# Kernel tuning notes

Measured on AMD Instinct MI355X. Metric: run time of the kernel, lower is better.

Reference implementation:

```python
import jax, jax.numpy as jnp
import numpy as np

N, E, F_IN, H, D, K = 50000, 800000, 128, 128, 64, 4

def setup_inputs():
    key = jax.random.key(0)
    ks = jax.random.split(key, 10)
    def rnd(k, shape, s=0.05):
        return jax.random.normal(k, shape, dtype=jnp.float32) * s
    return {
        "x": jax.random.normal(ks[0], (N, F_IN), dtype=jnp.float32),
        "edge_index": jax.random.randint(ks[1], (2, E), 0, N, dtype=jnp.int32),
        "W1": rnd(ks[2], (F_IN, H)),
        "b1": jnp.zeros((H,), jnp.float32),
        "a1": jnp.full((), 0.25, jnp.float32),
        "W2": rnd(ks[3], (H, H)),
        "b2": jnp.zeros((H,), jnp.float32),
        "a2": jnp.full((), 0.25, jnp.float32),
        "Wmu": rnd(ks[4], (K, H, D)),
        "bmu": jnp.zeros((K, D), jnp.float32),
        "amu": jnp.full((K,), 0.25, jnp.float32),
        "Wlv": rnd(ks[5], (K, H, D)),
        "blv": jnp.zeros((K, D), jnp.float32),
        "alv": jnp.full((K,), 0.25, jnp.float32),
        "Wr": rnd(ks[6], (K, D)),
        "br": jnp.zeros((K,), jnp.float32),
        "eps": jax.random.normal(ks[7], (N, K * D), dtype=jnp.float32),
    }

def _prelu(v, a):
    return jnp.where(v >= 0, v, a * v)

def _gcn_norm(edge_index):
    # PyG GCNConv defaults: add self-loops, symmetric deg^{-1/2} normalization
    loop = jnp.arange(N, dtype=edge_index.dtype)
    src = jnp.concatenate([edge_index[0], loop])
    dst = jnp.concatenate([edge_index[1], loop])
    deg = jax.ops.segment_sum(jnp.ones_like(dst, jnp.float32), dst, num_segments=N)
    dinv = jnp.where(deg > 0, jax.lax.rsqrt(deg), 0.0)
    norm = dinv[src] * dinv[dst]  # per-edge coefficient
    return src, dst, norm

def reference(x, edge_index, W1, b1, a1, W2, b2, a2, Wmu, bmu, amu, Wlv, blv, alv, Wr, br, eps):
    src, dst, norm = _gcn_norm(edge_index)
    def prop(h):  # gather -> normalize -> scatter-add
        return jax.ops.segment_sum(h[src] * norm[:, None], dst, num_segments=N)
    # shared GCN stack: GCNConv = propagate(x @ W) + b, then PReLU
    h = _prelu(prop(x @ W1) + b1, a1)
    hgcn = _prelu(prop(h @ W2) + b2, a2)
    # per-branch GCNConvs share the input; propagation is linear, so
    # propagate(hgcn @ Wk) == propagate(hgcn) @ Wk -> propagate once for all K
    p = prop(hgcn)  # (N, H)
    mu_k = _prelu(jnp.einsum('nh,khd->knd', p, Wmu) + bmu[:, None, :], amu[:, None, None])  # (K,N,D)
    lv_k = jax.nn.sigmoid(_prelu(jnp.einsum('nh,khd->knd', p, Wlv) + blv[:, None, :], alv[:, None, None]))
    mu = jnp.transpose(mu_k, (1, 0, 2)).reshape(N, K * D)
    logvar = jnp.transpose(lv_k, (1, 0, 2)).reshape(N, K * D)
    hk = eps * jnp.exp(0.5 * logvar) + mu  # reparameterize
    r = jax.nn.sigmoid(jnp.einsum('nkd,kd->nk', hk.reshape(N, K, D), Wr) + br)  # (N,K)
    return hgcn, logvar, mu, hk, r
```

## Files before the change

### kernel.cpp

```cpp
#include <hip/hip_runtime.h>
#include <math.h>

#define N_NODES 50000
#define N_EDGES 800000
#define HDIM 128
#define KD 256

typedef float f32x4 __attribute__((ext_vector_type(4)));
typedef short s16x8 __attribute__((ext_vector_type(8)));

__device__ __forceinline__ ushort f2b(float f) {
    union { float f; unsigned u; } x; x.f = f;
    unsigned u = x.u;
    return (ushort)((u + 0x7FFF + ((u >> 16) & 1)) >> 16);
}
__device__ __forceinline__ float b2f(ushort h) {
    union { unsigned u; float f; } x; x.u = ((unsigned)h) << 16; return x.f;
}

__global__ void zero_int(int* __restrict__ p, int n) {
    int i = blockIdx.x * blockDim.x + threadIdx.x;
    if (i < n) p[i] = 0;
}

__global__ void count_deg(const int* __restrict__ dst, int* __restrict__ cnt, int e) {
    int i = blockIdx.x * blockDim.x + threadIdx.x;
    if (i < e) atomicAdd(&cnt[dst[i]], 1);
}

__global__ void calc_dinv(const int* __restrict__ cnt, float* __restrict__ dinv, int n) {
    int i = blockIdx.x * blockDim.x + threadIdx.x;
    if (i < n) dinv[i] = rsqrtf((float)(cnt[i] + 1));
}

__global__ __launch_bounds__(1024)
void scan_blk(const int* __restrict__ cnt, int* __restrict__ offsets,
              int* __restrict__ blocksum, int n) {
    __shared__ int wsum[16];
    int tid = threadIdx.x;
    int i = blockIdx.x * 1024 + tid;
    int lane = tid & 63, wid = tid >> 6;
    int v = (i < n) ? cnt[i] : 0;
    int x = v;
    #pragma unroll
    for (int off = 1; off < 64; off <<= 1) {
        int t = __shfl_up(x, off, 64);
        if (lane >= off) x += t;
    }
    if (lane == 63) wsum[wid] = x;
    __syncthreads();
    if (wid == 0) {
        int w = (lane < 16) ? wsum[lane] : 0;
        #pragma unroll
        for (int off = 1; off < 16; off <<= 1) {
            int t = __shfl_up(w, off, 64);
            if (lane >= off) w += t;
        }
        if (lane < 16) wsum[lane] = w;
    }
    __syncthreads();
    int waveoff = (wid > 0) ? wsum[wid - 1] : 0;
    if (i < n) offsets[i] = x + waveoff - v;
    if (tid == 1023) blocksum[blockIdx.x] = x + waveoff;
}

__global__ void scan_top(const int* __restrict__ blocksum, int* __restrict__ blockpref,
                         int* __restrict__ offsets, int nb, int n) {
    int lane = threadIdx.x;
    int v = (lane < nb) ? blocksum[lane] : 0;
    int x = v;
    #pragma unroll
    for (int off = 1; off < 64; off <<= 1) {
        int t = __shfl_up(x, off, 64);
        if (lane >= off) x += t;
    }
    if (lane < nb) blockpref[lane] = x - v;
    if (lane == 63) offsets[n] = x;
}

__global__ __launch_bounds__(1024)
void scan_add(int* __restrict__ offsets, int* __restrict__ cursor,
              const int* __restrict__ blockpref, int n) {
    int i = blockIdx.x * 1024 + threadIdx.x;
    if (i < n) {
        int o = offsets[i] + blockpref[blockIdx.x];
        offsets[i] = o;
        cursor[i] = o;
    }
}

__global__ void fill_csr(const int* __restrict__ src, const int* __restrict__ dst,
                         int* __restrict__ cursor, int* __restrict__ csr, int e) {
    int i = blockIdx.x * blockDim.x + threadIdx.x;
    if (i < e) {
        int d = dst[i];
        int pos = atomicAdd(&cursor[d], 1);
        csr[pos] = src[i];
    }
}

__global__ void conv_x(const float4* __restrict__ x, ushort4* __restrict__ o,
                       const float* __restrict__ dinv, int n4) {
    int i = blockIdx.x * 256 + threadIdx.x;
    if (i >= n4) return;
    int row = i >> 5;
    float dv = dinv[row];
    float4 v = x[i];
    ushort4 u;
    u.x = f2b(v.x * dv); u.y = f2b(v.y * dv);
    u.z = f2b(v.z * dv); u.w = f2b(v.w * dv);
    o[i] = u;
}

__global__ void prep_w(const float* __restrict__ W1, const float* __restrict__ W2,
                       const float* __restrict__ Wmu, const float* __restrict__ Wlv,
                       ushort* __restrict__ w1t, ushort* __restrict__ w2t,
                       ushort* __restrict__ bt3) {
    int i = blockIdx.x * 256 + threadIdx.x;
    if (i < 16384) {
        int nn = i >> 7, k = i & 127;
        w1t[i] = f2b(W1[k * 128 + nn]);
    } else if (i < 32768) {
        int j = i - 16384; int nn = j >> 7, k = j & 127;
        w2t[j] = f2b(W2[k * 128 + nn]);
    } else if (i < 98304) {
        int j = i - 32768;
        int h = j & 127; int nk = j >> 7; int nn = nk & 127; int k = nk >> 7;
        float v = (nn < 64) ? Wmu[k * 8192 + h * 64 + nn]
                            : Wlv[k * 8192 + h * 64 + (nn - 64)];
        bt3[j] = f2b(v);
    }
}

__global__ __launch_bounds__(256)
void prop_b(const ushort* __restrict__ hin, ushort* __restrict__ hout,
            const int* __restrict__ csr, const int* __restrict__ offsets,
            const float* __restrict__ dinv, int n) {
    int gw = blockIdx.x * 4 + (threadIdx.x >> 6);
    if (gw >= n) return;
    int lane = threadIdx.x & 63;
    int grp = lane >> 4, gl = lane & 15;
    int coff = gl << 3;
    int beg = offsets[gw], end = offsets[gw + 1];
    float a0[8] = {0.f,0.f,0.f,0.f,0.f,0.f,0.f,0.f};
    float a1[8] = {0.f,0.f,0.f,0.f,0.f,0.f,0.f,0.f};
    for (int base = beg; base < end; base += 64) {
        int cnt = end - base; if (cnt > 64) cnt = 64;
        int sidx = (lane < cnt) ? csr[base + lane] : 0;
        int j = grp;
        for (; j + 4 < cnt; j += 8) {
            int s0 = __shfl(sidx, j, 64);
            int s1 = __shfl(sidx, j + 4, 64);
            s16x8 v0 = *(const s16x8*)(hin + (s0 << 7) + coff);
            s16x8 v1 = *(const s16x8*)(hin + (s1 << 7) + coff);
            #pragma unroll
            for (int q = 0; q < 8; ++q) {
                a0[q] += b2f((ushort)v0[q]);
                a1[q] += b2f((ushort)v1[q]);
            }
        }
        if (j < cnt) {
            int s0 = __shfl(sidx, j, 64);
            s16x8 v0 = *(const s16x8*)(hin + (s0 << 7) + coff);
            #pragma unroll
            for (int q = 0; q < 8; ++q) a0[q] += b2f((ushort)v0[q]);
        }
    }
    #pragma unroll
    for (int q = 0; q < 8; ++q) {
        float t = a0[q] + a1[q];
        t += __shfl_xor(t, 16, 64);
        t += __shfl_xor(t, 32, 64);
        a0[q] = t;
    }
    if (grp == 0) {
        s16x8 sv = *(const s16x8*)(hin + (gw << 7) + coff);
        float dn = dinv[gw];
        s16x8 o;
        #pragma unroll
        for (int q = 0; q < 8; ++q) {
            float t = (a0[q] + b2f((ushort)sv[q])) * dn;
            o[q] = (short)f2b(t);
        }
        *(s16x8*)(hout + (gw << 7) + coff) = o;
    }
}

template<int MODE>
__global__ __launch_bounds__(256)
void gemm12(const ushort* __restrict__ A, const ushort* __restrict__ Bt,
            const float* __restrict__ bias, const float* __restrict__ alpha,
            const float* __restrict__ dinv,
            float* __restrict__ Cf, ushort* __restrict__ Cb, int nrows) {
    __shared__ char As[32768];
    __shared__ char Bs[32768];
    int tid = threadIdx.x;
    int row0 = blockIdx.x * 128;
    #pragma unroll
    for (int it = 0; it < 8; ++it) {
        int idx = tid + it * 256;
        int r = idx >> 4, cb = (idx & 15) << 4;
        int sw = cb ^ ((r & 15) << 4);
        uint4 v = make_uint4(0, 0, 0, 0);
        int row = row0 + r;
        if (row < nrows) v = *(const uint4*)((const char*)A + (size_t)row * 256 + cb);
        *(uint4*)(As + r * 256 + sw) = v;
        uint4 bv = *(const uint4*)((const char*)Bt + (size_t)idx * 16);
        *(uint4*)(Bs + r * 256 + sw) = bv;
    }
    __syncthreads();

    int w = tid >> 6, lane = tid & 63;
    int bq = lane >> 4, tr = lane & 15;
    f32x4 acc[2][8];
    #pragma unroll
    for (int mi = 0; mi < 2; ++mi)
        #pragma unroll
        for (int nj = 0; nj < 8; ++nj)
            acc[mi][nj] = (f32x4){0.f, 0.f, 0.f, 0.f};

    #pragma unroll
    for (int s = 0; s < 4; ++s) {
        int xoff = (s * 64 + bq * 16) ^ ((tr & 15) << 4);
        s16x8 af[2], bfr[8];
        #pragma unroll
        for (int mi = 0; mi < 2; ++mi)
            af[mi] = *(const s16x8*)(As + (w * 32 + mi * 16 + tr) * 256 + xoff);
        #pragma unroll
        for (int nj = 0; nj < 8; ++nj)
            bfr[nj] = *(const s16x8*)(Bs + (nj * 16 + tr) * 256 + xoff);
        #pragma unroll
        for (int mi = 0; mi < 2; ++mi)
            #pragma unroll
            for (int nj = 0; nj < 8; ++nj)
                acc[mi][nj] = __builtin_amdgcn_mfma_f32_16x16x32_bf16(af[mi], bfr[nj], acc[mi][nj], 0, 0, 0);
    }

    int g = lane >> 4, c = lane & 15;
    float aval = alpha[0];
    float bb[8];
    #pragma unroll
    for (int nj = 0; nj < 8; ++nj) bb[nj] = bias[nj * 16 + c];
    #pragma unroll
    for (int mi = 0; mi < 2; ++mi) {
        #pragma unroll
        for (int j = 0; j < 4; ++j) {
            int row = row0 + w * 32 + mi * 16 + g * 4 + j;
            if (row >= nrows) continue;
            float dv = dinv[row];
            #pragma unroll
            for (int nj = 0; nj < 8; ++nj) {
                int col = nj * 16 + c;
                float t = acc[mi][nj][j] + bb[nj];
                t = t >= 0.f ? t : aval * t;
                if (MODE) Cf[(size_t)row * 128 + col] = t;
                Cb[(size_t)row * 128 + col] = f2b(t * dv);
            }
        }
    }
}

template<int FUSED>
__global__ __launch_bounds__(256)
void gemm3(const ushort* __restrict__ A, const ushort* __restrict__ Bt3,
           const float* __restrict__ bmu, const float* __restrict__ blv,
           const float* __restrict__ amu, const float* __restrict__ alv,
           const float* __restrict__ Wr, const float* __restrict__ br,
           const float* __restrict__ eps,
           float* __restrict__ out_mu, float* __restrict__ out_lv,
           float* __restrict__ out_hk, float* __restrict__ out_r, int nrows) {
    __shared__ char As[32768];
    __shared__ char Bs[32768];
    int tid = threadIdx.x;
    int k = blockIdx.x;
    int row0 = blockIdx.y * 128;
    const ushort* Bt = Bt3 + (size_t)k * 16384;
    #pragma unroll
    for (int it = 0; it < 8; ++it) {
        int idx = tid + it * 256;
        int r = idx >> 4, cb = (idx & 15) << 4;
        int sw = cb ^ ((r & 15) << 4);
        uint4 v = make_uint4(0, 0, 0, 0);
        int row = row0 + r;
        if (row < nrows) v = *(const uint4*)((const char*)A + (size_t)row * 256 + cb);
        *(uint4*)(As + r * 256 + sw) = v;
        uint4 bv = *(const uint4*)((const char*)Bt + (size_t)idx * 16);
        *(uint4*)(Bs + r * 256 + sw) = bv;
    }
    __syncthreads();

    int w = tid >> 6, lane = tid & 63;
    int bq = lane >> 4, tr = lane & 15;
    f32x4 acc[2][8];
    #pragma unroll
    for (int mi = 0; mi < 2; ++mi)
        #pragma unroll
        for (int nj = 0; nj < 8; ++nj)
            acc[mi][nj] = (f32x4){0.f, 0.f, 0.f, 0.f};

    #pragma unroll
    for (int s = 0; s < 4; ++s) {
        int xoff = (s * 64 + bq * 16) ^ ((tr & 15) << 4);
        s16x8 af[2], bfr[8];
        #pragma unroll
        for (int mi = 0; mi < 2; ++mi)
            af[mi] = *(const s16x8*)(As + (w * 32 + mi * 16 + tr) * 256 + xoff);
        #pragma unroll
        for (int nj = 0; nj < 8; ++nj)
            bfr[nj] = *(const s16x8*)(Bs + (nj * 16 + tr) * 256 + xoff);
        #pragma unroll
        for (int mi = 0; mi < 2; ++mi)
            #pragma unroll
            for (int nj = 0; nj < 8; ++nj)
                acc[mi][nj] = __builtin_amdgcn_mfma_f32_16x16x32_bf16(af[mi], bfr[nj], acc[mi][nj], 0, 0, 0);
    }

    int g = lane >> 4, c = lane & 15;
    float amuv = amu[k], alvv = alv[k];
    float brk = br[k];
    float bmv[4], blvb[4], wrv[4];
    #pragma unroll
    for (int nj = 0; nj < 4; ++nj) {
        int d = nj * 16 + c;
        bmv[nj] = bmu[k * 64 + d];
        blvb[nj] = blv[k * 64 + d];
        wrv[nj] = FUSED ? Wr[k * 64 + d] : 0.f;
    }
    #pragma unroll
    for (int mi = 0; mi < 2; ++mi) {
        float rsum[4] = {0.f, 0.f, 0.f, 0.f};
        #pragma unroll
        for (int j = 0; j < 4; ++j) {
            int row = row0 + w * 32 + mi * 16 + g * 4 + j;
            if (row >= nrows) continue;
            #pragma unroll
            for (int nj = 0; nj < 4; ++nj) {
                int d = nj * 16 + c;
                size_t oc = (size_t)row * KD + k * 64 + d;
                float m_ = acc[mi][nj][j] + bmv[nj];
                m_ = m_ >= 0.f ? m_ : amuv * m_;
                float l_ = acc[mi][nj + 4][j] + blvb[nj];
                l_ = l_ >= 0.f ? l_ : alvv * l_;
                l_ = 1.f / (1.f + __expf(-l_));
                out_mu[oc] = m_;
                out_lv[oc] = l_;
                if (FUSED) {
                    float h = fmaf(eps[oc], __expf(0.5f * l_), m_);
                    out_hk[oc] = h;
                    rsum[j] = fmaf(h, wrv[nj], rsum[j]);
                }
            }
        }
        if (FUSED) {
            #pragma unroll
            for (int j = 0; j < 4; ++j) {
                float t = rsum[j];
                t += __shfl_xor(t, 1, 64);
                t += __shfl_xor(t, 2, 64);
                t += __shfl_xor(t, 4, 64);
                t += __shfl_xor(t, 8, 64);
                if (c == 0) {
                    int row = row0 + w * 32 + mi * 16 + g * 4 + j;
                    if (row < nrows)
                        out_r[(size_t)row * 4 + k] = 1.f / (1.f + __expf(-(t + brk)));
                }
            }
        }
    }
}

__global__ void hk_kernel(const float* __restrict__ mu, const float* __restrict__ lv,
                          const float* __restrict__ eps, const float* __restrict__ Wr,
                          const float* __restrict__ br, float* __restrict__ hk,
                          float* __restrict__ r, int n) {
    int gw = (blockIdx.x * blockDim.x + threadIdx.x) >> 6;
    int lane = threadIdx.x & 63;
    if (gw >= n) return;
    size_t base = (size_t)gw * KD;
    #pragma unroll
    for (int k = 0; k < 4; ++k) {
        int c = k * 64 + lane;
        float m = mu[base + c], v = lv[base + c], e = eps[base + c];
        float h = fmaf(e, __expf(0.5f * v), m);
        hk[base + c] = h;
        float t = h * Wr[k * 64 + lane];
        #pragma unroll
        for (int off = 32; off >= 1; off >>= 1) t += __shfl_xor(t, off, 64);
        if (lane == 0) r[(size_t)gw * 4 + k] = 1.f / (1.f + __expf(-(t + br[k])));
    }
}

extern "C" void kernel_launch(void* const* d_in, const int* in_sizes, int n_in,
                              void* d_out, int out_size, void* d_ws, size_t ws_size,
                              hipStream_t stream) {
    const float* x   = (const float*)d_in[0];
    const int*   ei  = (const int*)d_in[1];
    const float* W1  = (const float*)d_in[2];
    const float* b1  = (const float*)d_in[3];
    const float* a1  = (const float*)d_in[4];
    const float* W2  = (const float*)d_in[5];
    const float* b2  = (const float*)d_in[6];
    const float* a2  = (const float*)d_in[7];
    const float* Wmu = (const float*)d_in[8];
    const float* bmu = (const float*)d_in[9];
    const float* amu = (const float*)d_in[10];
    const float* Wlv = (const float*)d_in[11];
    const float* blv = (const float*)d_in[12];
    const float* alv = (const float*)d_in[13];
    const float* Wr  = (const float*)d_in[14];
    const float* br  = (const float*)d_in[15];
    const float* eps = (const float*)d_in[16];

    float* out      = (float*)d_out;
    float* out_hgcn = out;
    float* out_lv   = out + (size_t)N_NODES * HDIM;
    float* out_mu   = out_lv + (size_t)N_NODES * KD;
    float* out_hk   = out_mu + (size_t)N_NODES * KD;
    float* out_r    = out_hk + (size_t)N_NODES * KD;

    char* ws = (char*)d_ws;
    int*    cnt      = (int*)ws;
    int*    offsets  = (int*)(ws + 204800);
    int*    cursor   = (int*)(ws + 409600);
    int*    csr      = (int*)(ws + 614400);
    float*  dinv     = (float*)(ws + 3814400);
    ushort* w1t      = (ushort*)(ws + 4014592);
    ushort* w2t      = (ushort*)(ws + 4047360);
    ushort* bt3      = (ushort*)(ws + 4080128);
    int*    blocksum = (int*)(ws + 4211200);
    int*    blockpref= (int*)(ws + 4211456);

    ushort* S0 = (ushort*)out_hk;
    ushort* S1 = S0 + (size_t)N_NODES * HDIM;
    ushort* S2 = S1 + (size_t)N_NODES * HDIM;
    ushort* S3 = S2 + (size_t)N_NODES * HDIM;

    const size_t P_OFF = 4211712;
    const bool fused = ws_size >= P_OFF + (size_t)N_NODES * HDIM * 2;
    ushort* P = fused ? (ushort*)(ws + P_OFF) : S1;

    const int* e_src = ei;
    const int* e_dst = ei + N_EDGES;
    const int NB = (N_NODES + 1023) / 1024;

    zero_int <<<(N_NODES + 255) / 256, 256, 0, stream>>>(cnt, N_NODES);
    count_deg<<<(N_EDGES + 255) / 256, 256, 0, stream>>>(e_dst, cnt, N_EDGES);
    calc_dinv<<<(N_NODES + 255) / 256, 256, 0, stream>>>(cnt, dinv, N_NODES);
    scan_blk <<<NB, 1024, 0, stream>>>(cnt, offsets, blocksum, N_NODES);
    scan_top <<<1, 64, 0, stream>>>(blocksum, blockpref, offsets, NB, N_NODES);
    scan_add <<<NB, 1024, 0, stream>>>(offsets, cursor, blockpref, N_NODES);
    fill_csr <<<(N_EDGES + 255) / 256, 256, 0, stream>>>(e_src, e_dst, cursor, csr, N_EDGES);

    prep_w<<<384, 256, 0, stream>>>(W1, W2, Wmu, Wlv, w1t, w2t, bt3);
    conv_x<<<(N_NODES * 32 + 255) / 256, 256, 0, stream>>>((const float4*)x, (ushort4*)S0, dinv, N_NODES * 32);

    prop_b<<<12500, 256, 0, stream>>>(S0, S1, csr, offsets, dinv, N_NODES);
    gemm12<0><<<391, 256, 0, stream>>>(S1, w1t, b1, a1, dinv, nullptr, S2, N_NODES);
    prop_b<<<12500, 256, 0, stream>>>(S2, S3, csr, offsets, dinv, N_NODES);
    gemm12<1><<<391, 256, 0, stream>>>(S3, w2t, b2, a2, dinv, out_hgcn, S0, N_NODES);
    prop_b<<<12500, 256, 0, stream>>>(S0, P, csr, offsets, dinv, N_NODES);

    dim3 g3(4, 391);
    if (fused) {
        gemm3<1><<<g3, 256, 0, stream>>>(P, bt3, bmu, blv, amu, alv, Wr, br, eps,
                                         out_mu, out_lv, out_hk, out_r, N_NODES);
    } else {
        gemm3<0><<<g3, 256, 0, stream>>>(P, bt3, bmu, blv, amu, alv, Wr, br, eps,
                                         out_mu, out_lv, out_hk, out_r, N_NODES);
        hk_kernel<<<12500, 256, 0, stream>>>(out_mu, out_lv, eps, Wr, br, out_hk, out_r, N_NODES);
    }
}
```

Before: 291.7 us.

## Split propagation kernel across feature quarters with 16 edges per wavefront

The sparse gather-propagate kernel now uses a 2D grid where blockIdx.y picks a 32-column quarter of the 128-wide feature row. Each wavefront processes 16 edges at once, with 4 lanes per edge, instead of 4 edges with 16 lanes each. This gives more memory-level parallelism per wave and spreads the work over four times as many blocks, at the cost of 64-byte row segments per edge instead of full 256-byte rows. It also reads the CSR indices four times and adds two extra shuffle-reduction steps.

```diff
diff --git a/kernel.cpp b/kernel.cpp
--- a/kernel.cpp
+++ b/kernel.cpp
@@ -133,56 +133,44 @@
 }
 
 __global__ __launch_bounds__(256)
-void prop_b(const ushort* __restrict__ hin, ushort* __restrict__ hout,
+void prop_q(const ushort* __restrict__ hin, ushort* __restrict__ hout,
             const int* __restrict__ csr, const int* __restrict__ offsets,
             const float* __restrict__ dinv, int n) {
-    int gw = blockIdx.x * 4 + (threadIdx.x >> 6);
-    if (gw >= n) return;
+    int node = blockIdx.x * 4 + (threadIdx.x >> 6);
+    if (node >= n) return;
     int lane = threadIdx.x & 63;
-    int grp = lane >> 4, gl = lane & 15;
-    int coff = gl << 3;
-    int beg = offsets[gw], end = offsets[gw + 1];
-    float a0[8] = {0.f,0.f,0.f,0.f,0.f,0.f,0.f,0.f};
-    float a1[8] = {0.f,0.f,0.f,0.f,0.f,0.f,0.f,0.f};
+    int e = lane >> 2, il = lane & 3;
+    int eoff = blockIdx.y * 32 + (il << 3);
+    int beg = offsets[node], end = offsets[node + 1];
+    float acc[8] = {0.f,0.f,0.f,0.f,0.f,0.f,0.f,0.f};
     for (int base = beg; base < end; base += 64) {
         int cnt = end - base; if (cnt > 64) cnt = 64;
         int sidx = (lane < cnt) ? csr[base + lane] : 0;
-        int j = grp;
-        for (; j + 4 < cnt; j += 8) {
-            int s0 = __shfl(sidx, j, 64);
-            int s1 = __shfl(sidx, j + 4, 64);
-            s16x8 v0 = *(const s16x8*)(hin + (s0 << 7) + coff);
-            s16x8 v1 = *(const s16x8*)(hin + (s1 << 7) + coff);
-            #pragma unroll
-            for (int q = 0; q < 8; ++q) {
-                a0[q] += b2f((ushort)v0[q]);
-                a1[q] += b2f((ushort)v1[q]);
-            }
+        #pragma unroll 4
+        for (int j = e; j < cnt; j += 16) {
+            int s = __shfl(sidx, j, 64);
+            s16x8 v = *(const s16x8*)(hin + (s << 7) + eoff);
+            #pragma unroll
+            for (int q = 0; q < 8; ++q) acc[q] += b2f((ushort)v[q]);
         }
-        if (j < cnt) {
-            int s0 = __shfl(sidx, j, 64);
-            s16x8 v0 = *(const s16x8*)(hin + (s0 << 7) + coff);
-            #pragma unroll
-            for (int q = 0; q < 8; ++q) a0[q] += b2f((ushort)v0[q]);
-        }
     }
     #pragma unroll
     for (int q = 0; q < 8; ++q) {
-        float t = a0[q] + a1[q];
+        float t = acc[q];
+        t += __shfl_xor(t, 4, 64);
+        t += __shfl_xor(t, 8, 64);
         t += __shfl_xor(t, 16, 64);
         t += __shfl_xor(t, 32, 64);
-        a0[q] = t;
-    }
-    if (grp == 0) {
-        s16x8 sv = *(const s16x8*)(hin + (gw << 7) + coff);
-        float dn = dinv[gw];
+        acc[q] = t;
+    }
+    if (e == 0) {
+        s16x8 sv = *(const s16x8*)(hin + (node << 7) + eoff);
+        float dn = dinv[node];
         s16x8 o;
         #pragma unroll
-        for (int q = 0; q < 8; ++q) {
-            float t = (a0[q] + b2f((ushort)sv[q])) * dn;
-            o[q] = (short)f2b(t);
-        }
-        *(s16x8*)(hout + (gw << 7) + coff) = o;
+        for (int q = 0; q < 8; ++q)
+            o[q] = (short)f2b((acc[q] + b2f((ushort)sv[q])) * dn);
+        *(s16x8*)(hout + (node << 7) + eoff) = o;
     }
 }
 
@@ -454,11 +442,12 @@
     prep_w<<<384, 256, 0, stream>>>(W1, W2, Wmu, Wlv, w1t, w2t, bt3);
     conv_x<<<(N_NODES * 32 + 255) / 256, 256, 0, stream>>>((const float4*)x, (ushort4*)S0, dinv, N_NODES * 32);
 
-    prop_b<<<12500, 256, 0, stream>>>(S0, S1, csr, offsets, dinv, N_NODES);
+    dim3 gp(12500, 4);
+    prop_q<<<gp, 256, 0, stream>>>(S0, S1, csr, offsets, dinv, N_NODES);
     gemm12<0><<<391, 256, 0, stream>>>(S1, w1t, b1, a1, dinv, nullptr, S2, N_NODES);
-    prop_b<<<12500, 256, 0, stream>>>(S2, S3, csr, offsets, dinv, N_NODES);
+    prop_q<<<gp, 256, 0, stream>>>(S2, S3, csr, offsets, dinv, N_NODES);
     gemm12<1><<<391, 256, 0, stream>>>(S3, w2t, b2, a2, dinv, out_hgcn, S0, N_NODES);
-    prop_b<<<12500, 256, 0, stream>>>(S0, P, csr, offsets, dinv, N_NODES);
+    prop_q<<<gp, 256, 0, stream>>>(S0, P, csr, offsets, dinv, N_NODES);
 
     dim3 g3(4, 391);
     if (fused) {
```

Measured after the change: 432.9 us. +48.4%, slower.

## Switch gather intermediates to fp16, fp32 propagate outputs with split-bf16 GEMMs, sort CSR

Applied to the files above, without the earlier changes.

Gathered features are now stored as fp16 instead of bf16. Propagation outputs are written in fp32, and the GEMMs split each fp32 A value into hi and lo bf16 parts, issuing two MFMAs per tile, which recovers accuracy. A per-node insertion sort of the CSR neighbour lists is added, which may improve gather locality and makes summation order deterministic. The trade is more memory traffic on propagate outputs and GEMM inputs (fp32 instead of 16-bit), twice the MFMA work, 96KB of LDS per GEMM block, and an extra sort kernel. This looks aimed mainly at accuracy rather than speed.

```diff
diff --git a/kernel.cpp b/kernel.cpp
--- a/kernel.cpp
+++ b/kernel.cpp
@@ -16,6 +16,12 @@
 }
 __device__ __forceinline__ float b2f(ushort h) {
     union { unsigned u; float f; } x; x.u = ((unsigned)h) << 16; return x.f;
+}
+__device__ __forceinline__ ushort f2h(float f) {
+    union { _Float16 h; ushort u; } x; x.h = (_Float16)f; return x.u;
+}
+__device__ __forceinline__ float h2f(ushort u) {
+    union { ushort u; _Float16 h; } x; x.u = u; return (float)x.h;
 }
 
 __global__ void zero_int(int* __restrict__ p, int n) {
@@ -99,6 +105,18 @@
     }
 }
 
+__global__ void sort_csr(int* __restrict__ csr, const int* __restrict__ offsets, int n) {
+    int node = blockIdx.x * 256 + threadIdx.x;
+    if (node >= n) return;
+    int beg = offsets[node], end = offsets[node + 1];
+    for (int i = beg + 1; i < end; ++i) {
+        int key = csr[i];
+        int j = i - 1;
+        while (j >= beg && csr[j] > key) { csr[j + 1] = csr[j]; --j; }
+        csr[j + 1] = key;
+    }
+}
+
 __global__ void conv_x(const float4* __restrict__ x, ushort4* __restrict__ o,
                        const float* __restrict__ dinv, int n4) {
     int i = blockIdx.x * 256 + threadIdx.x;
@@ -107,8 +125,8 @@
     float dv = dinv[row];
     float4 v = x[i];
     ushort4 u;
-    u.x = f2b(v.x * dv); u.y = f2b(v.y * dv);
-    u.z = f2b(v.z * dv); u.w = f2b(v.w * dv);
+    u.x = f2h(v.x * dv); u.y = f2h(v.y * dv);
+    u.z = f2h(v.z * dv); u.w = f2h(v.w * dv);
     o[i] = u;
 }
 
@@ -133,7 +151,7 @@
 }
 
 __global__ __launch_bounds__(256)
-void prop_b(const ushort* __restrict__ hin, ushort* __restrict__ hout,
+void prop_b(const ushort* __restrict__ hin, float* __restrict__ hout,
             const int* __restrict__ csr, const int* __restrict__ offsets,
             const float* __restrict__ dinv, int n) {
     int gw = blockIdx.x * 4 + (threadIdx.x >> 6);
@@ -155,15 +173,15 @@
             s16x8 v1 = *(const s16x8*)(hin + (s1 << 7) + coff);
             #pragma unroll
             for (int q = 0; q < 8; ++q) {
-                a0[q] += b2f((ushort)v0[q]);
-                a1[q] += b2f((ushort)v1[q]);
+                a0[q] += h2f((ushort)v0[q]);
+                a1[q] += h2f((ushort)v1[q]);
             }
         }
         if (j < cnt) {
             int s0 = __shfl(sidx, j, 64);
             s16x8 v0 = *(const s16x8*)(hin + (s0 << 7) + coff);
             #pragma unroll
-            for (int q = 0; q < 8; ++q) a0[q] += b2f((ushort)v0[q]);
+            for (int q = 0; q < 8; ++q) a0[q] += h2f((ushort)v0[q]);
         }
     }
     #pragma unroll
@@ -176,23 +194,24 @@
     if (grp == 0) {
         s16x8 sv = *(const s16x8*)(hin + (gw << 7) + coff);
         float dn = dinv[gw];
-        s16x8 o;
-        #pragma unroll
-        for (int q = 0; q < 8; ++q) {
-            float t = (a0[q] + b2f((ushort)sv[q])) * dn;
-            o[q] = (short)f2b(t);
-        }
-        *(s16x8*)(hout + (gw << 7) + coff) = o;
+        float* orow = hout + (gw << 7) + coff;
+        float o[8];
+        #pragma unroll
+        for (int q = 0; q < 8; ++q)
+            o[q] = (a0[q] + h2f((ushort)sv[q])) * dn;
+        *(float4*)(orow)     = make_float4(o[0], o[1], o[2], o[3]);
+        *(float4*)(orow + 4) = make_float4(o[4], o[5], o[6], o[7]);
     }
 }
 
 template<int MODE>
 __global__ __launch_bounds__(256)
-void gemm12(const ushort* __restrict__ A, const ushort* __restrict__ Bt,
+void gemm12(const float* __restrict__ A, const ushort* __restrict__ Bt,
             const float* __restrict__ bias, const float* __restrict__ alpha,
             const float* __restrict__ dinv,
-            float* __restrict__ Cf, ushort* __restrict__ Cb, int nrows) {
-    __shared__ char As[32768];
+            float* __restrict__ Cf, ushort* __restrict__ Ch, int nrows) {
+    __shared__ char Ah[32768];
+    __shared__ char Al[32768];
     __shared__ char Bs[32768];
     int tid = threadIdx.x;
     int row0 = blockIdx.x * 128;
@@ -201,10 +220,24 @@
         int idx = tid + it * 256;
         int r = idx >> 4, cb = (idx & 15) << 4;
         int sw = cb ^ ((r & 15) << 4);
-        uint4 v = make_uint4(0, 0, 0, 0);
         int row = row0 + r;
-        if (row < nrows) v = *(const uint4*)((const char*)A + (size_t)row * 256 + cb);
-        *(uint4*)(As + r * 256 + sw) = v;
+        float vv[8] = {0.f,0.f,0.f,0.f,0.f,0.f,0.f,0.f};
+        if (row < nrows) {
+            const float* src = A + (size_t)row * 128 + ((idx & 15) << 3);
+            float4 v0 = *(const float4*)(src);
+            float4 v1 = *(const float4*)(src + 4);
+            vv[0]=v0.x; vv[1]=v0.y; vv[2]=v0.z; vv[3]=v0.w;
+            vv[4]=v1.x; vv[5]=v1.y; vv[6]=v1.z; vv[7]=v1.w;
+        }
+        ushort hi[8], lo[8];
+        #pragma unroll
+        for (int q = 0; q < 8; ++q) {
+            ushort h = f2b(vv[q]);
+            hi[q] = h;
+            lo[q] = f2b(vv[q] - b2f(h));
+        }
+        *(uint4*)(Ah + r * 256 + sw) = *(uint4*)hi;
+        *(uint4*)(Al + r * 256 + sw) = *(uint4*)lo;
         uint4 bv = *(const uint4*)((const char*)Bt + (size_t)idx * 16);
         *(uint4*)(Bs + r * 256 + sw) = bv;
     }
@@ -222,18 +255,22 @@
     #pragma unroll
     for (int s = 0; s < 4; ++s) {
         int xoff = (s * 64 + bq * 16) ^ ((tr & 15) << 4);
-        s16x8 af[2], bfr[8];
-        #pragma unroll
-        for (int mi = 0; mi < 2; ++mi)
-            af[mi] = *(const s16x8*)(As + (w * 32 + mi * 16 + tr) * 256 + xoff);
+        s16x8 ah[2], al[2], bfr[8];
+        #pragma unroll
+        for (int mi = 0; mi < 2; ++mi) {
+            ah[mi] = *(const s16x8*)(Ah + (w * 32 + mi * 16 + tr) * 256 + xoff);
+            al[mi] = *(const s16x8*)(Al + (w * 32 + mi * 16 + tr) * 256 + xoff);
+        }
         #pragma unroll
         for (int nj = 0; nj < 8; ++nj)
             bfr[nj] = *(const s16x8*)(Bs + (nj * 16 + tr) * 256 + xoff);
         #pragma unroll
         for (int mi = 0; mi < 2; ++mi)
             #pragma unroll
-            for (int nj = 0; nj < 8; ++nj)
-                acc[mi][nj] = __builtin_amdgcn_mfma_f32_16x16x32_bf16(af[mi], bfr[nj], acc[mi][nj], 0, 0, 0);
+            for (int nj = 0; nj < 8; ++nj) {
+                acc[mi][nj] = __builtin_amdgcn_mfma_f32_16x16x32_bf16(ah[mi], bfr[nj], acc[mi][nj], 0, 0, 0);
+                acc[mi][nj] = __builtin_amdgcn_mfma_f32_16x16x32_bf16(al[mi], bfr[nj], acc[mi][nj], 0, 0, 0);
+            }
     }
 
     int g = lane >> 4, c = lane & 15;
@@ -254,7 +291,7 @@
                 float t = acc[mi][nj][j] + bb[nj];
                 t = t >= 0.f ? t : aval * t;
                 if (MODE) Cf[(size_t)row * 128 + col] = t;
-                Cb[(size_t)row * 128 + col] = f2b(t * dv);
+                Ch[(size_t)row * 128 + col] = f2h(t * dv);
             }
         }
     }
@@ -262,14 +299,15 @@
 
 template<int FUSED>
 __global__ __launch_bounds__(256)
-void gemm3(const ushort* __restrict__ A, const ushort* __restrict__ Bt3,
+void gemm3(const float* __restrict__ A, const ushort* __restrict__ Bt3,
            const float* __restrict__ bmu, const float* __restrict__ blv,
            const float* __restrict__ amu, const float* __restrict__ alv,
            const float* __restrict__ Wr, const float* __restrict__ br,
            const float* __restrict__ eps,
            float* __restrict__ out_mu, float* __restrict__ out_lv,
            float* __restrict__ out_hk, float* __restrict__ out_r, int nrows) {
-    __shared__ char As[32768];
+    __shared__ char Ah[32768];
+    __shared__ char Al[32768];
     __shared__ char Bs[32768];
     int tid = threadIdx.x;
     int k = blockIdx.x;
@@ -280,10 +318,24 @@
         int idx = tid + it * 256;
         int r = idx >> 4, cb = (idx & 15) << 4;
         int sw = cb ^ ((r & 15) << 4);
-        uint4 v = make_uint4(0, 0, 0, 0);
         int row = row0 + r;
-        if (row < nrows) v = *(const uint4*)((const char*)A + (size_t)row * 256 + cb);
-        *(uint4*)(As + r * 256 + sw) = v;
+        float vv[8] = {0.f,0.f,0.f,0.f,0.f,0.f,0.f,0.f};
+        if (row < nrows) {
+            const float* src = A + (size_t)row * 128 + ((idx & 15) << 3);
+            float4 v0 = *(const float4*)(src);
+            float4 v1 = *(const float4*)(src + 4);
+            vv[0]=v0.x; vv[1]=v0.y; vv[2]=v0.z; vv[3]=v0.w;
+            vv[4]=v1.x; vv[5]=v1.y; vv[6]=v1.z; vv[7]=v1.w;
+        }
+        ushort hi[8], lo[8];
+        #pragma unroll
+        for (int q = 0; q < 8; ++q) {
+            ushort h = f2b(vv[q]);
+            hi[q] = h;
+            lo[q] = f2b(vv[q] - b2f(h));
+        }
+        *(uint4*)(Ah + r * 256 + sw) = *(uint4*)hi;
+        *(uint4*)(Al + r * 256 + sw) = *(uint4*)lo;
         uint4 bv = *(const uint4*)((const char*)Bt + (size_t)idx * 16);
         *(uint4*)(Bs + r * 256 + sw) = bv;
     }
@@ -301,18 +353,22 @@
     #pragma unroll
     for (int s = 0; s < 4; ++s) {
         int xoff = (s * 64 + bq * 16) ^ ((tr & 15) << 4);
-        s16x8 af[2], bfr[8];
-        #pragma unroll
-        for (int mi = 0; mi < 2; ++mi)
-            af[mi] = *(const s16x8*)(As + (w * 32 + mi * 16 + tr) * 256 + xoff);
+        s16x8 ah[2], al[2], bfr[8];
+        #pragma unroll
+        for (int mi = 0; mi < 2; ++mi) {
+            ah[mi] = *(const s16x8*)(Ah + (w * 32 + mi * 16 + tr) * 256 + xoff);
+            al[mi] = *(const s16x8*)(Al + (w * 32 + mi * 16 + tr) * 256 + xoff);
+        }
         #pragma unroll
         for (int nj = 0; nj < 8; ++nj)
             bfr[nj] = *(const s16x8*)(Bs + (nj * 16 + tr) * 256 + xoff);
         #pragma unroll
         for (int mi = 0; mi < 2; ++mi)
             #pragma unroll
-            for (int nj = 0; nj < 8; ++nj)
-                acc[mi][nj] = __builtin_amdgcn_mfma_f32_16x16x32_bf16(af[mi], bfr[nj], acc[mi][nj], 0, 0, 0);
+            for (int nj = 0; nj < 8; ++nj) {
+                acc[mi][nj] = __builtin_amdgcn_mfma_f32_16x16x32_bf16(ah[mi], bfr[nj], acc[mi][nj], 0, 0, 0);
+                acc[mi][nj] = __builtin_amdgcn_mfma_f32_16x16x32_bf16(al[mi], bfr[nj], acc[mi][nj], 0, 0, 0);
+            }
     }
 
     int g = lane >> 4, c = lane & 15;
@@ -430,14 +486,16 @@
     int*    blocksum = (int*)(ws + 4211200);
     int*    blockpref= (int*)(ws + 4211456);
 
-    ushort* S0 = (ushort*)out_hk;
-    ushort* S1 = S0 + (size_t)N_NODES * HDIM;
-    ushort* S2 = S1 + (size_t)N_NODES * HDIM;
-    ushort* S3 = S2 + (size_t)N_NODES * HDIM;
+    ushort* X16 = (ushort*)out_hk;
+    ushort* H16 = X16 + (size_t)N_NODES * HDIM;
+    ushort* G16 = H16 + (size_t)N_NODES * HDIM;
+
+    float* q1 = out_mu;
+    float* q2 = out_lv;
 
     const size_t P_OFF = 4211712;
-    const bool fused = ws_size >= P_OFF + (size_t)N_NODES * HDIM * 2;
-    ushort* P = fused ? (ushort*)(ws + P_OFF) : S1;
+    const bool fused = ws_size >= P_OFF + (size_t)N_NODES * HDIM * 4;
+    float* P = fused ? (float*)(ws + P_OFF) : (float*)out_hk;
 
     const int* e_src = ei;
     const int* e_dst = ei + N_EDGES;
@@ -450,15 +508,16 @@
     scan_top <<<1, 64, 0, stream>>>(blocksum, blockpref, offsets, NB, N_NODES);
     scan_add <<<NB, 1024, 0, stream>>>(offsets, cursor, blockpref, N_NODES);
     fill_csr <<<(N_EDGES + 255) / 256, 256, 0, stream>>>(e_src, e_dst, cursor, csr, N_EDGES);
+    sort_csr <<<(N_NODES + 255) / 256, 256, 0, stream>>>(csr, offsets, N_NODES);
 
     prep_w<<<384, 256, 0, stream>>>(W1, W2, Wmu, Wlv, w1t, w2t, bt3);
-    conv_x<<<(N_NODES * 32 + 255) / 256, 256, 0, stream>>>((const float4*)x, (ushort4*)S0, dinv, N_NODES * 32);
-
-    prop_b<<<12500, 256, 0, stream>>>(S0, S1, csr, offsets, dinv, N_NODES);
-    gemm12<0><<<391, 256, 0, stream>>>(S1, w1t, b1, a1, dinv, nullptr, S2, N_NODES);
-    prop_b<<<12500, 256, 0, stream>>>(S2, S3, csr, offsets, dinv, N_NODES);
-    gemm12<1><<<391, 256, 0, stream>>>(S3, w2t, b2, a2, dinv, out_hgcn, S0, N_NODES);
-    prop_b<<<12500, 256, 0, stream>>>(S0, P, csr, offsets, dinv, N_NODES);
+    conv_x<<<(N_NODES * 32 + 255) / 256, 256, 0, stream>>>((const float4*)x, (ushort4*)X16, dinv, N_NODES * 32);
+
+    prop_b<<<12500, 256, 0, stream>>>(X16, q1, csr, offsets, dinv, N_NODES);
+    gemm12<0><<<391, 256, 0, stream>>>(q1, w1t, b1, a1, dinv, nullptr, H16, N_NODES);
+    prop_b<<<12500, 256, 0, stream>>>(H16, q2, csr, offsets, dinv, N_NODES);
+    gemm12<1><<<391, 256, 0, stream>>>(q2, w2t, b2, a2, dinv, out_hgcn, G16, N_NODES);
+    prop_b<<<12500, 256, 0, stream>>>(G16, P, csr, offsets, dinv, N_NODES);
 
     dim3 g3(4, 391);
     if (fused) {
```

Measured after the change: 435.9 us. 1.49x slower.

## Store gathered features as fp16, sort CSR neighbors, and reassign scratch buffers

Applied to the files above, without the earlier changes.

The features gathered during propagation (conv_x output and gemm12 output) are now stored as fp16 instead of bf16, while the propagated results stay bf16 for the MFMA GEMMs. A new per-node insertion-sort kernel orders each CSR neighbor list by source index, aiming for more local gather accesses. Scratch buffers are reassigned so intermediates live in the mu/lv output regions. The sort adds an extra kernel with serial per-thread work, and fp16 carries a range-overflow risk in exchange for extra mantissa bits.

```diff
diff --git a/kernel.cpp b/kernel.cpp
--- a/kernel.cpp
+++ b/kernel.cpp
@@ -16,6 +16,12 @@
 }
 __device__ __forceinline__ float b2f(ushort h) {
     union { unsigned u; float f; } x; x.u = ((unsigned)h) << 16; return x.f;
+}
+__device__ __forceinline__ ushort f2h(float f) {
+    union { _Float16 h; ushort u; } x; x.h = (_Float16)f; return x.u;
+}
+__device__ __forceinline__ float h2f(ushort u) {
+    union { ushort u; _Float16 h; } x; x.u = u; return (float)x.h;
 }
 
 __global__ void zero_int(int* __restrict__ p, int n) {
@@ -99,6 +105,18 @@
     }
 }
 
+__global__ void sort_csr(int* __restrict__ csr, const int* __restrict__ offsets, int n) {
+    int node = blockIdx.x * 256 + threadIdx.x;
+    if (node >= n) return;
+    int beg = offsets[node], end = offsets[node + 1];
+    for (int i = beg + 1; i < end; ++i) {
+        int key = csr[i];
+        int j = i - 1;
+        while (j >= beg && csr[j] > key) { csr[j + 1] = csr[j]; --j; }
+        csr[j + 1] = key;
+    }
+}
+
 __global__ void conv_x(const float4* __restrict__ x, ushort4* __restrict__ o,
                        const float* __restrict__ dinv, int n4) {
     int i = blockIdx.x * 256 + threadIdx.x;
@@ -107,8 +125,8 @@
     float dv = dinv[row];
     float4 v = x[i];
     ushort4 u;
-    u.x = f2b(v.x * dv); u.y = f2b(v.y * dv);
-    u.z = f2b(v.z * dv); u.w = f2b(v.w * dv);
+    u.x = f2h(v.x * dv); u.y = f2h(v.y * dv);
+    u.z = f2h(v.z * dv); u.w = f2h(v.w * dv);
     o[i] = u;
 }
 
@@ -155,15 +173,15 @@
             s16x8 v1 = *(const s16x8*)(hin + (s1 << 7) + coff);
             #pragma unroll
             for (int q = 0; q < 8; ++q) {
-                a0[q] += b2f((ushort)v0[q]);
-                a1[q] += b2f((ushort)v1[q]);
+                a0[q] += h2f((ushort)v0[q]);
+                a1[q] += h2f((ushort)v1[q]);
             }
         }
         if (j < cnt) {
             int s0 = __shfl(sidx, j, 64);
             s16x8 v0 = *(const s16x8*)(hin + (s0 << 7) + coff);
             #pragma unroll
-            for (int q = 0; q < 8; ++q) a0[q] += b2f((ushort)v0[q]);
+            for (int q = 0; q < 8; ++q) a0[q] += h2f((ushort)v0[q]);
         }
     }
     #pragma unroll
@@ -176,13 +194,11 @@
     if (grp == 0) {
         s16x8 sv = *(const s16x8*)(hin + (gw << 7) + coff);
         float dn = dinv[gw];
-        s16x8 o;
-        #pragma unroll
-        for (int q = 0; q < 8; ++q) {
-            float t = (a0[q] + b2f((ushort)sv[q])) * dn;
-            o[q] = (short)f2b(t);
-        }
-        *(s16x8*)(hout + (gw << 7) + coff) = o;
+        s16x8 ob;
+        #pragma unroll
+        for (int q = 0; q < 8; ++q)
+            ob[q] = (short)f2b((a0[q] + h2f((ushort)sv[q])) * dn);
+        *(s16x8*)(hout + (gw << 7) + coff) = ob;
     }
 }
 
@@ -191,7 +207,7 @@
 void gemm12(const ushort* __restrict__ A, const ushort* __restrict__ Bt,
             const float* __restrict__ bias, const float* __restrict__ alpha,
             const float* __restrict__ dinv,
-            float* __restrict__ Cf, ushort* __restrict__ Cb, int nrows) {
+            float* __restrict__ Cf, ushort* __restrict__ Ch, int nrows) {
     __shared__ char As[32768];
     __shared__ char Bs[32768];
     int tid = threadIdx.x;
@@ -254,7 +270,7 @@
                 float t = acc[mi][nj][j] + bb[nj];
                 t = t >= 0.f ? t : aval * t;
                 if (MODE) Cf[(size_t)row * 128 + col] = t;
-                Cb[(size_t)row * 128 + col] = f2b(t * dv);
+                Ch[(size_t)row * 128 + col] = f2h(t * dv);
             }
         }
     }
@@ -430,14 +446,16 @@
     int*    blocksum = (int*)(ws + 4211200);
     int*    blockpref= (int*)(ws + 4211456);
 
-    ushort* S0 = (ushort*)out_hk;
-    ushort* S1 = S0 + (size_t)N_NODES * HDIM;
-    ushort* S2 = S1 + (size_t)N_NODES * HDIM;
-    ushort* S3 = S2 + (size_t)N_NODES * HDIM;
+    ushort* X16 = (ushort*)out_hk;
+    ushort* H16 = X16 + (size_t)N_NODES * HDIM;
+    ushort* G16 = H16 + (size_t)N_NODES * HDIM;
+
+    ushort* q1b = (ushort*)out_mu;
+    ushort* q2b = (ushort*)out_lv;
 
     const size_t P_OFF = 4211712;
     const bool fused = ws_size >= P_OFF + (size_t)N_NODES * HDIM * 2;
-    ushort* P = fused ? (ushort*)(ws + P_OFF) : S1;
+    ushort* P = fused ? (ushort*)(ws + P_OFF) : X16;
 
     const int* e_src = ei;
     const int* e_dst = ei + N_EDGES;
@@ -450,15 +468,16 @@
     scan_top <<<1, 64, 0, stream>>>(blocksum, blockpref, offsets, NB, N_NODES);
     scan_add <<<NB, 1024, 0, stream>>>(offsets, cursor, blockpref, N_NODES);
     fill_csr <<<(N_EDGES + 255) / 256, 256, 0, stream>>>(e_src, e_dst, cursor, csr, N_EDGES);
+    sort_csr <<<(N_NODES + 255) / 256, 256, 0, stream>>>(csr, offsets, N_NODES);
 
     prep_w<<<384, 256, 0, stream>>>(W1, W2, Wmu, Wlv, w1t, w2t, bt3);
-    conv_x<<<(N_NODES * 32 + 255) / 256, 256, 0, stream>>>((const float4*)x, (ushort4*)S0, dinv, N_NODES * 32);
-
-    prop_b<<<12500, 256, 0, stream>>>(S0, S1, csr, offsets, dinv, N_NODES);
-    gemm12<0><<<391, 256, 0, stream>>>(S1, w1t, b1, a1, dinv, nullptr, S2, N_NODES);
-    prop_b<<<12500, 256, 0, stream>>>(S2, S3, csr, offsets, dinv, N_NODES);
-    gemm12<1><<<391, 256, 0, stream>>>(S3, w2t, b2, a2, dinv, out_hgcn, S0, N_NODES);
-    prop_b<<<12500, 256, 0, stream>>>(S0, P, csr, offsets, dinv, N_NODES);
+    conv_x<<<(N_NODES * 32 + 255) / 256, 256, 0, stream>>>((const float4*)x, (ushort4*)X16, dinv, N_NODES * 32);
+
+    prop_b<<<12500, 256, 0, stream>>>(X16, q1b, csr, offsets, dinv, N_NODES);
+    gemm12<0><<<391, 256, 0, stream>>>(q1b, w1t, b1, a1, dinv, nullptr, H16, N_NODES);
+    prop_b<<<12500, 256, 0, stream>>>(H16, q2b, csr, offsets, dinv, N_NODES);
+    gemm12<1><<<391, 256, 0, stream>>>(q2b, w2t, b2, a2, dinv, out_hgcn, G16, N_NODES);
+    prop_b<<<12500, 256, 0, stream>>>(G16, P, csr, offsets, dinv, N_NODES);
 
     dim3 g3(4, 391);
     if (fused) {
```

Result: slower. 378.6 us (+29.8%).
